# Kernel tuning notes

Measured on AMD Instinct MI355X. Metric: run time of the kernel, lower is better.

## Reference

```python
import jax, jax.numpy as jnp
import numpy as np
import math

EPS = 1e-6          # eps for safe cumprod / clamping
CHUNK = 4           # chunk_size w
SHARP = 1.0         # sharpening_factor
NOISE_STD = 1.0
N_HEADS = 4
ADIM = 512


def moving_sum(x, back, forward):
    """Windowed running sum over last axis: out[k] = sum_{j=k-back}^{k+forward} x[j].
    Equivalent to the conv1d trick in the original (all-ones filter)."""
    k = x.shape[-1]
    pad = [(0, 0)] * (x.ndim - 1) + [(back, forward)]
    c = jnp.cumsum(jnp.pad(x, pad), axis=-1)
    c0 = jnp.concatenate([jnp.zeros_like(c[..., :1]), c], axis=-1)
    w = back + forward
    return c0[..., w + 1: w + 1 + k] - c0[..., :k]


def setup_inputs() -> dict:
    rng = jax.random.key(0)
    ks = jax.random.split(rng, 12)
    B, qlen, klen, kdim, qdim, adim = 8, 256, 2048, 512, 512, ADIM
    s = 0.02
    return {
        "key_enc": jax.random.normal(ks[0], (B, klen, kdim), jnp.float32),
        "query":   jax.random.normal(ks[1], (B, qlen, qdim), jnp.float32),
        "noise":   jax.random.normal(ks[2], (B, qlen, klen), jnp.float32),
        # monotonic energy params
        "Wk_m": jax.random.normal(ks[3], (kdim, adim), jnp.float32) * s,
        "bk_m": jnp.zeros((adim,), jnp.float32),
        "Wq_m": jax.random.normal(ks[4], (qdim, adim), jnp.float32) * s,
        "bq_m": jnp.zeros((adim,), jnp.float32),
        "r":    jnp.array([-4.0], jnp.float32),
        # chunkwise energy params (multi-head)
        "Wk_c": jax.random.normal(ks[5], (kdim, adim), jnp.float32) * s,
        "bk_c": jnp.zeros((adim,), jnp.float32),
        "Wq_c": jax.random.normal(ks[6], (qdim, adim), jnp.float32) * s,
        "bq_c": jnp.zeros((adim,), jnp.float32),
    }


def _mocha_beta(key_enc, query, noise, Wk_m, bk_m, Wq_m, bq_m, r,
                Wk_c, bk_c, Wq_c, bq_c):
    B, klen, _ = key_enc.shape
    qlen = query.shape[1]
    H = N_HEADS
    dk = ADIM // H
    scale = math.sqrt(ADIM)

    # --- monotonic energy (single head): [B, qlen, klen]
    k_m = key_enc @ Wk_m + bk_m
    q_m = query @ Wq_m + bq_m
    e_mono = jnp.einsum('bqa,bka->bqk', q_m, k_m) / scale + r[0]

    # --- p_choose with additive gaussian noise (encourages discreteness)
    p_choose = jax.nn.sigmoid(e_mono + noise * NOISE_STD)  # [B,q,k]

    # --- safe cumprod of (1 - p) via exclusive cumsum in log space
    log1mp = jnp.log(jnp.clip(1.0 - p_choose, EPS, 1.0))
    cumprod_1mp = jnp.exp(jnp.cumsum(log1mp, axis=-1) - log1mp)  # exclusive

    # --- monotonic alpha recurrence over query steps (parallel-mode MoChA)
    aw0 = jnp.zeros((B, klen), jnp.float32).at[:, 0].set(1.0)

    def step(aw_prev, inp):
        p_i, cp_i = inp  # [B, klen]
        alpha_i = p_i * cp_i * jnp.cumsum(
            aw_prev / jnp.clip(cp_i, EPS, 1.0), axis=-1)
        return alpha_i, alpha_i

    xs = (jnp.swapaxes(p_choose, 0, 1), jnp.swapaxes(cumprod_1mp, 0, 1))
    _, alpha_q = jax.lax.scan(step, aw0, xs)          # [q, B, k]
    alpha = jnp.swapaxes(alpha_q, 0, 1)                # [B, q, k]

    # --- chunkwise energy (multi-head): [B, H, q, k]
    k_c = (key_enc @ Wk_c + bk_c).reshape(B, klen, H, dk)
    q_c = (query @ Wq_c + bq_c).reshape(B, qlen, H, dk)
    e_chunk = jnp.einsum('bqhd,bkhd->bhqk', q_c, k_c) / scale

    # --- efficient chunkwise attention (clipped-logit moving-sum softmax)
    e = e_chunk - jnp.max(e_chunk, axis=3, keepdims=True)
    softmax_exp = jnp.maximum(jnp.exp(e), 1e-5)
    denom = moving_sum(softmax_exp, back=CHUNK - 1, forward=0)
    beta = softmax_exp * moving_sum(
        alpha[:, None] * SHARP / denom, back=0, forward=CHUNK - 1)
    return beta  # [B, H, q, k]


def reference(key_enc, query, noise, Wk_m, bk_m, Wq_m, bq_m, r,
              Wk_c, bk_c, Wq_c, bq_c):
    return _mocha_beta(key_enc, query, noise, Wk_m, bk_m, Wq_m, bq_m, r,
                       Wk_c, bk_c, Wq_c, bq_c)
```

## Files before the change

kernel.cpp:

```cpp
#include <hip/hip_runtime.h>
#include <math.h>

#define BATCH   8
#define QLEN    256
#define KLEN    2048
#define KDIM    512
#define ADIMC   512
#define NHEADS  4
#define DKH     128
#define CHUNKW  4

static constexpr float INV_SCALE = 0.04419417382415922f;
static constexpr float EPSV = 1e-6f;

typedef __attribute__((ext_vector_type(8))) short bf16x8;
typedef __attribute__((ext_vector_type(4))) float f32x4;

__device__ __forceinline__ unsigned short f2bf(float f) {
    unsigned u = __builtin_bit_cast(unsigned, f);
    u += 0x7fffu + ((u >> 16) & 1u);
    return (unsigned short)(u >> 16);
}

__device__ __forceinline__ void lds_barrier() {
    __asm__ volatile("s_waitcnt lgkmcnt(0)\n\ts_barrier" ::: "memory");
}

__device__ __forceinline__ void gload_lds16(const void* g, void* l) {
    __builtin_amdgcn_global_load_lds(
        (const __attribute__((address_space(1))) void*)g,
        (__attribute__((address_space(3))) void*)l, 16, 0, 0);
}

__global__ __launch_bounds__(256) void cast_bf16(
    const float* __restrict__ x, unsigned short* __restrict__ y, int n4)
{
    int i = blockIdx.x * 256 + threadIdx.x;
    if (i < n4) {
        float4 v = ((const float4*)x)[i];
        ushort4 o;
        o.x = f2bf(v.x); o.y = f2bf(v.y); o.z = f2bf(v.z); o.w = f2bf(v.w);
        ((ushort4*)y)[i] = o;
    }
}

__global__ __launch_bounds__(256) void transpose_cast(
    const float* __restrict__ W, unsigned short* __restrict__ WT)
{
    __shared__ float tile[32][33];
    const int tx = threadIdx.x;
    const int ty = threadIdx.y;
    const int k0 = blockIdx.y * 32, n0 = blockIdx.x * 32;
    #pragma unroll
    for (int i = 0; i < 32; i += 8)
        tile[ty + i][tx] = W[(size_t)(k0 + ty + i) * KDIM + n0 + tx];
    __syncthreads();
    #pragma unroll
    for (int i = 0; i < 32; i += 8)
        WT[(size_t)(n0 + ty + i) * KDIM + k0 + tx] = f2bf(tile[tx][ty + i]);
}

template<int KSTEPS>
__device__ __forceinline__ void mfma_nt_staged(
    const unsigned short* __restrict__ A, const unsigned short* __restrict__ B,
    int lda, int ldb, int bm, int bn,
    unsigned short* AsLDS, unsigned short* BsLDS, f32x4 acc[4][4])
{
    const int t = threadIdx.x;
    const int wv = t >> 6, ln = t & 63;
    const int r = ln & 15, quad = ln >> 4;
    const int wm = (wv >> 1) * 64, wn = (wv & 1) * 64;
    const int srow = wv * 16 + (ln >> 2);
    const int scol = (ln & 3) * 8;

    for (int ks = 0; ks < KSTEPS; ++ks) {
        const int k0 = ks * 32;
        #pragma unroll
        for (int j = 0; j < 2; ++j) {
            gload_lds16(A + (size_t)(bm + j * 64 + srow) * lda + k0 + scol,
                        AsLDS + (size_t)(j * 64 + wv * 16) * 32);
            gload_lds16(B + (size_t)(bn + j * 64 + srow) * ldb + k0 + scol,
                        BsLDS + (size_t)(j * 64 + wv * 16) * 32);
        }
        __syncthreads();
        bf16x8 af[4], bg[4];
        #pragma unroll
        for (int f = 0; f < 4; ++f)
            af[f] = *(const bf16x8*)(AsLDS + (size_t)(wm + f * 16 + r) * 32 + quad * 8);
        #pragma unroll
        for (int f = 0; f < 4; ++f)
            bg[f] = *(const bf16x8*)(BsLDS + (size_t)(wn + f * 16 + r) * 32 + quad * 8);
        #pragma unroll
        for (int i = 0; i < 4; ++i)
            #pragma unroll
            for (int j2 = 0; j2 < 4; ++j2)
                acc[i][j2] = __builtin_amdgcn_mfma_f32_16x16x32_bf16(
                    af[i], bg[j2], acc[i][j2], 0, 0, 0);
        __syncthreads();
    }
}

__device__ __forceinline__ void zero_acc(f32x4 acc[4][4]) {
    #pragma unroll
    for (int i = 0; i < 4; ++i)
        #pragma unroll
        for (int j = 0; j < 4; ++j)
            acc[i][j] = f32x4{0.f, 0.f, 0.f, 0.f};
}

__global__ __launch_bounds__(256) void proj_mfma(
    const unsigned short* __restrict__ A, const unsigned short* __restrict__ WT,
    const float* __restrict__ bias_m, const float* __restrict__ bias_c,
    unsigned short* __restrict__ C)
{
    __shared__ unsigned short As[128 * 32];
    __shared__ unsigned short Bs[128 * 32];
    const int bm = blockIdx.y * 128, bn = blockIdx.x * 128;
    f32x4 acc[4][4]; zero_acc(acc);
    mfma_nt_staged<16>(A, WT, KDIM, KDIM, bm, bn, As, Bs, acc);
    const int wv = threadIdx.x >> 6, ln = threadIdx.x & 63;
    const int r = ln & 15, quad = ln >> 4;
    const int m0 = bm + (wv >> 1) * 64, n0 = bn + (wv & 1) * 64;
    #pragma unroll
    for (int j = 0; j < 4; ++j) {
        const int n = n0 + j * 16 + r;
        const float bv = (n < 512) ? bias_m[n] : bias_c[n - 512];
        #pragma unroll
        for (int i = 0; i < 4; ++i) {
            #pragma unroll
            for (int reg = 0; reg < 4; ++reg) {
                const int m = m0 + i * 16 + quad * 4 + reg;
                C[(size_t)m * 1024 + n] = f2bf(acc[i][j][reg] + bv);
            }
        }
    }
}

__global__ __launch_bounds__(256) void pchoose_mfma(
    const unsigned short* __restrict__ qp, const unsigned short* __restrict__ kp,
    const float* __restrict__ noise, const float* __restrict__ rp,
    float* __restrict__ p)
{
    __shared__ unsigned short As[128 * 32];
    __shared__ unsigned short Bs[128 * 32];
    const int b = blockIdx.z;
    const unsigned short* A = qp + (size_t)b * QLEN * 1024;
    const unsigned short* B = kp + (size_t)b * KLEN * 1024;
    const int bm = blockIdx.y * 128, bn = blockIdx.x * 128;
    f32x4 acc[4][4]; zero_acc(acc);
    mfma_nt_staged<16>(A, B, 1024, 1024, bm, bn, As, Bs, acc);
    const int wv = threadIdx.x >> 6, ln = threadIdx.x & 63;
    const int r = ln & 15, quad = ln >> 4;
    const int m0 = bm + (wv >> 1) * 64, n0 = bn + (wv & 1) * 64;
    const float rv = rp[0];
    #pragma unroll
    for (int i = 0; i < 4; ++i) {
        #pragma unroll
        for (int reg = 0; reg < 4; ++reg) {
            const int q = m0 + i * 16 + quad * 4 + reg;
            const size_t rowoff = ((size_t)b * QLEN + q) * KLEN;
            #pragma unroll
            for (int j = 0; j < 4; ++j) {
                const int k = n0 + j * 16 + r;
                const float e = acc[i][j][reg] * INV_SCALE + rv + noise[rowoff + k];
                p[rowoff + k] = __builtin_amdgcn_rcpf(1.0f + __expf(-e));
            }
        }
    }
}

__device__ __forceinline__ float wave_incl_scan(float x)
{
#define DPP_ADD(ctrl, rmask, bctrl)                                            \
    { int _t = __builtin_amdgcn_update_dpp(0, __builtin_bit_cast(int, x),      \
                                           ctrl, rmask, 0xf, bctrl);           \
      x += __builtin_bit_cast(float, _t); }
    DPP_ADD(0x111, 0xf, true)
    DPP_ADD(0x112, 0xf, true)
    DPP_ADD(0x114, 0xf, true)
    DPP_ADD(0x118, 0xf, true)
    DPP_ADD(0x142, 0xa, false)
    DPP_ADD(0x143, 0xc, false)
#undef DPP_ADD
    return x;
}

__global__ __launch_bounds__(256) void cumprod_mr(
    const float* __restrict__ p, float* __restrict__ mArr, float* __restrict__ rArr)
{
    const size_t row = blockIdx.x;
    const float* pr = p + row * KLEN;
    float* mr = mArr + row * KLEN;
    float* rr = rArr + row * KLEN;
    const int tid = threadIdx.x;
    const int lane = tid & 63, wid = tid >> 6;
    __shared__ float waveTot[4];

    float4 v0 = *(const float4*)(pr + tid * 8);
    float4 v1 = *(const float4*)(pr + tid * 8 + 4);
    float pv[8] = {v0.x, v0.y, v0.z, v0.w, v1.x, v1.y, v1.z, v1.w};
    float excl[8];
    float run = 0.0f;
    #pragma unroll
    for (int j = 0; j < 8; ++j) {
        float l = __logf(fminf(fmaxf(1.0f - pv[j], EPSV), 1.0f));
        excl[j] = run;
        run += l;
    }
    float s = wave_incl_scan(run);
    if (lane == 63) waveTot[wid] = s;
    __syncthreads();
    float wex = 0.0f;
    for (int w = 0; w < wid; ++w) wex += waveTot[w];
    const float texcl = wex + s - run;

    float mv[8], rv[8];
    #pragma unroll
    for (int j = 0; j < 8; ++j) {
        const float cpv = __expf(texcl + excl[j]);
        mv[j] = pv[j] * cpv;
        rv[j] = __builtin_amdgcn_rcpf(fminf(fmaxf(cpv, EPSV), 1.0f));
    }
    *(float4*)(mr + tid * 8)     = *(float4*)&mv[0];
    *(float4*)(mr + tid * 8 + 4) = *(float4*)&mv[4];
    *(float4*)(rr + tid * 8)     = *(float4*)&rv[0];
    *(float4*)(rr + tid * 8 + 4) = *(float4*)&rv[4];
}

__global__ __launch_bounds__(512, 1) void alpha_echunk(
    const float* __restrict__ mArr, const float* __restrict__ rArr,
    float* __restrict__ alpha,
    const unsigned short* __restrict__ qp, const unsigned short* __restrict__ kp,
    float* __restrict__ out)
{
    __shared__ __align__(16) char smem[16384];
    const int bid = blockIdx.x;
    const int tid = threadIdx.x;

    if (bid < BATCH) {
        float (*wt)[8] = (float (*)[8])smem;
        const int lane = tid & 63, wid = tid >> 6;
        const float* mrow = mArr + (size_t)bid * QLEN * KLEN + tid * 4;
        const float* rrow = rArr + (size_t)bid * QLEN * KLEN + tid * 4;
        float* arow = alpha + (size_t)bid * QLEN * KLEN + tid * 4;

        float aw0 = 0.f, aw1 = 0.f, aw2 = 0.f, aw3 = 0.f;
        if (tid == 0) aw0 = 1.0f;

        float4 mA = *(const float4*)(mrow);
        float4 rA = *(const float4*)(rrow);
        float4 mB = *(const float4*)(mrow + KLEN);
        float4 rB = *(const float4*)(rrow + KLEN);

#define ASTEP(I, MREG, RREG)                                                   \
    {                                                                          \
        const int i_ = (I);                                                    \
        float4 mc = MREG, rc = RREG;                                           \
        const int rn_ = (i_ + 2 < QLEN) ? (i_ + 2) : (QLEN - 1);               \
        MREG = *(const float4*)(mrow + (size_t)rn_ * KLEN);                    \
        RREG = *(const float4*)(rrow + (size_t)rn_ * KLEN);                    \
        float run = 0.0f, i0, i1, i2, i3;                                      \
        run = fmaf(aw0, rc.x, run); i0 = run;                                  \
        run = fmaf(aw1, rc.y, run); i1 = run;                                  \
        run = fmaf(aw2, rc.z, run); i2 = run;                                  \
        run = fmaf(aw3, rc.w, run); i3 = run;                                  \
        float tot = wave_incl_scan(run);                                       \
        if (lane == 63) wt[i_ & 1][wid] = tot;                                 \
        lds_barrier();                                                         \
        float base = tot - run;                                                \
        float4 w0 = *(const float4*)&wt[i_ & 1][0];                            \
        float4 w1 = *(const float4*)&wt[i_ & 1][4];                            \
        if (wid > 0) base += w0.x;                                             \
        if (wid > 1) base += w0.y;                                             \
        if (wid > 2) base += w0.z;                                             \
        if (wid > 3) base += w0.w;                                             \
        if (wid > 4) base += w1.x;                                             \
        if (wid > 5) base += w1.y;                                             \
        if (wid > 6) base += w1.z;                                             \
        aw0 = mc.x * (base + i0);                                              \
        aw1 = mc.y * (base + i1);                                              \
        aw2 = mc.z * (base + i2);                                              \
        aw3 = mc.w * (base + i3);                                              \
        float4 ov; ov.x = aw0; ov.y = aw1; ov.z = aw2; ov.w = aw3;             \
        *(float4*)(arow + (size_t)i_ * KLEN) = ov;                             \
    }

        for (int io = 0; io < QLEN; io += 2) {
            ASTEP(io + 0, mA, rA)
            ASTEP(io + 1, mB, rB)
        }
#undef ASTEP
        return;
    }

    const int v = bid - BATCH;
    const int z = v >> 5;
    const int by = (v >> 4) & 1;
    const int bx = v & 15;
    const int b = z >> 2, h = z & 3;
    const bool worker = tid < 256;
    unsigned short* As = (unsigned short*)smem;
    unsigned short* Bs = (unsigned short*)(smem + 8192);
    const unsigned short* A = qp + (size_t)b * QLEN * 1024 + 512 + h * DKH;
    const unsigned short* B = kp + (size_t)b * KLEN * 1024 + 512 + h * DKH;
    const int bm = by * 128, bn = bx * 128;

    const int wv = tid >> 6, ln = tid & 63;
    const int r = ln & 15, quad = ln >> 4;
    const int wm = (wv >> 1) * 64, wn = (wv & 1) * 64;
    const int srow = (wv & 3) * 16 + (ln >> 2);
    const int scol = (ln & 3) * 8;

    f32x4 acc[4][4]; zero_acc(acc);
    for (int ks = 0; ks < 4; ++ks) {
        const int k0 = ks * 32;
        if (worker) {
            #pragma unroll
            for (int j = 0; j < 2; ++j) {
                gload_lds16(A + (size_t)(bm + j * 64 + srow) * 1024 + k0 + scol,
                            As + (size_t)(j * 64 + wv * 16) * 32);
                gload_lds16(B + (size_t)(bn + j * 64 + srow) * 1024 + k0 + scol,
                            Bs + (size_t)(j * 64 + wv * 16) * 32);
            }
        }
        __syncthreads();
        if (worker) {
            bf16x8 af[4], bg[4];
            #pragma unroll
            for (int f = 0; f < 4; ++f)
                af[f] = *(const bf16x8*)(As + (size_t)(wm + f * 16 + r) * 32 + quad * 8);
            #pragma unroll
            for (int f = 0; f < 4; ++f)
                bg[f] = *(const bf16x8*)(Bs + (size_t)(wn + f * 16 + r) * 32 + quad * 8);
            #pragma unroll
            for (int i = 0; i < 4; ++i)
                #pragma unroll
                for (int j2 = 0; j2 < 4; ++j2)
                    acc[i][j2] = __builtin_amdgcn_mfma_f32_16x16x32_bf16(
                        af[i], bg[j2], acc[i][j2], 0, 0, 0);
        }
        __syncthreads();
    }
    if (worker) {
        const int m0 = bm + (wv >> 1) * 64, n0 = bn + (wv & 1) * 64;
        #pragma unroll
        for (int i = 0; i < 4; ++i) {
            #pragma unroll
            for (int reg = 0; reg < 4; ++reg) {
                const int q = m0 + i * 16 + quad * 4 + reg;
                const size_t rowoff = ((size_t)z * QLEN + q) * KLEN;
                #pragma unroll
                for (int j = 0; j < 4; ++j) {
                    const int k = n0 + j * 16 + r;
                    out[rowoff + k] = acc[i][j][reg] * INV_SCALE;
                }
            }
        }
    }
}

__global__ __launch_bounds__(256) void beta_kernel(
    float* __restrict__ eo, const float* __restrict__ alpha)
{
    __shared__ float sse[KLEN + 3];
    __shared__ float su[KLEN + 3];
    __shared__ float wmax[4];

    const int tid = threadIdx.x;
    const int lane = tid & 63, wid = tid >> 6;
    const int row = blockIdx.x;
    const int q = row & (QLEN - 1);
    const int b = row >> 10;
    float* erow = eo + (size_t)row * KLEN;
    const float* arow = alpha + ((size_t)b * QLEN + q) * KLEN;

    if (tid < 3) { sse[tid] = 0.0f; su[KLEN + tid] = 0.0f; }

    float ev[8];
    float lm = -INFINITY;
    #pragma unroll
    for (int j = 0; j < 8; ++j) {
        const int k = tid + 256 * j;
        ev[j] = erow[k];
        lm = fmaxf(lm, ev[j]);
    }
    #pragma unroll
    for (int off = 32; off > 0; off >>= 1) lm = fmaxf(lm, __shfl_xor(lm, off));
    if (lane == 0) wmax[wid] = lm;
    __syncthreads();
    const float mx = fmaxf(fmaxf(wmax[0], wmax[1]), fmaxf(wmax[2], wmax[3]));

    #pragma unroll
    for (int j = 0; j < 8; ++j) {
        const int k = tid + 256 * j;
        sse[k + 3] = fmaxf(__expf(ev[j] - mx), 1e-5f);
    }
    __syncthreads();

    #pragma unroll
    for (int j = 0; j < 8; ++j) {
        const int k = tid + 256 * j;
        const float denom = sse[k + 3] + sse[k + 2] + sse[k + 1] + sse[k];
        su[k] = arow[k] * __builtin_amdgcn_rcpf(denom);
    }
    __syncthreads();

    #pragma unroll
    for (int j = 0; j < 8; ++j) {
        const int k = tid + 256 * j;
        erow[k] = sse[k + 3] * (su[k] + su[k + 1] + su[k + 2] + su[k + 3]);
    }
}

extern "C" void kernel_launch(void* const* d_in, const int* in_sizes, int n_in,
                              void* d_out, int out_size, void* d_ws, size_t ws_size,
                              hipStream_t stream)
{
    (void)in_sizes; (void)n_in; (void)out_size; (void)ws_size;
    const float* key_enc = (const float*)d_in[0];
    const float* query   = (const float*)d_in[1];
    const float* noise   = (const float*)d_in[2];
    const float* Wk_m    = (const float*)d_in[3];
    const float* bk_m    = (const float*)d_in[4];
    const float* Wq_m    = (const float*)d_in[5];
    const float* bq_m    = (const float*)d_in[6];
    const float* rp      = (const float*)d_in[7];
    const float* Wk_c    = (const float*)d_in[8];
    const float* bk_c    = (const float*)d_in[9];
    const float* Wq_c    = (const float*)d_in[10];
    const float* bq_c    = (const float*)d_in[11];
    float* out = (float*)d_out;

    char* w = (char*)d_ws;
    unsigned short* kx    = (unsigned short*)w; w += (size_t)BATCH * KLEN * KDIM * 2;
    unsigned short* qx    = (unsigned short*)w; w += (size_t)BATCH * QLEN * KDIM * 2;
    unsigned short* WTk   = (unsigned short*)w; w += (size_t)1024 * KDIM * 2;
    unsigned short* WTq   = (unsigned short*)w; w += (size_t)1024 * KDIM * 2;
    unsigned short* kproj = (unsigned short*)w; w += (size_t)BATCH * KLEN * 1024 * 2;
    unsigned short* qproj = (unsigned short*)w; w += (size_t)BATCH * QLEN * 1024 * 2;
    float* p_alpha = (float*)w; w += (size_t)BATCH * QLEN * KLEN * 4;
    float* mArr    = (float*)w; w += (size_t)BATCH * QLEN * KLEN * 4;
    float* rArr    = (float*)w;

    hipLaunchKernelGGL(cast_bf16, dim3(BATCH * KLEN * KDIM / 4 / 256), dim3(256), 0, stream,
                       key_enc, kx, BATCH * KLEN * KDIM / 4);
    hipLaunchKernelGGL(cast_bf16, dim3(BATCH * QLEN * KDIM / 4 / 256), dim3(256), 0, stream,
                       query, qx, BATCH * QLEN * KDIM / 4);
    hipLaunchKernelGGL(transpose_cast, dim3(16, 16), dim3(32, 8), 0, stream, Wk_m, WTk);
    hipLaunchKernelGGL(transpose_cast, dim3(16, 16), dim3(32, 8), 0, stream, Wk_c, WTk + (size_t)512 * KDIM);
    hipLaunchKernelGGL(transpose_cast, dim3(16, 16), dim3(32, 8), 0, stream, Wq_m, WTq);
    hipLaunchKernelGGL(transpose_cast, dim3(16, 16), dim3(32, 8), 0, stream, Wq_c, WTq + (size_t)512 * KDIM);

    hipLaunchKernelGGL(proj_mfma, dim3(8, BATCH * KLEN / 128), dim3(256), 0, stream,
                       kx, WTk, bk_m, bk_c, kproj);
    hipLaunchKernelGGL(proj_mfma, dim3(8, BATCH * QLEN / 128), dim3(256), 0, stream,
                       qx, WTq, bq_m, bq_c, qproj);

    hipLaunchKernelGGL(pchoose_mfma, dim3(KLEN / 128, QLEN / 128, BATCH), dim3(256), 0, stream,
                       qproj, kproj, noise, rp, p_alpha);

    hipLaunchKernelGGL(cumprod_mr, dim3(BATCH * QLEN), dim3(256), 0, stream,
                       p_alpha, mArr, rArr);

    hipLaunchKernelGGL(alpha_echunk, dim3(BATCH + KLEN / 128 * QLEN / 128 * BATCH * NHEADS),
                       dim3(512), 0, stream,
                       mArr, rArr, p_alpha, qproj, kproj, out);

    hipLaunchKernelGGL(beta_kernel, dim3(BATCH * NHEADS * QLEN), dim3(256), 0, stream,
                       out, p_alpha);
}
```

Measured before the change: 313.6 us.

## Run alpha scan with a single wave per batch to drop block barriers

After: 1.008 ms. 221% more time.

```diff
diff --git a/kernel.cpp b/kernel.cpp
--- a/kernel.cpp
+++ b/kernel.cpp
@@ -20,10 +20,6 @@
     unsigned u = __builtin_bit_cast(unsigned, f);
     u += 0x7fffu + ((u >> 16) & 1u);
     return (unsigned short)(u >> 16);
-}
-
-__device__ __forceinline__ void lds_barrier() {
-    __asm__ volatile("s_waitcnt lgkmcnt(0)\n\ts_barrier" ::: "memory");
 }
 
 __device__ __forceinline__ void gload_lds16(const void* g, void* l) {
@@ -238,58 +234,103 @@
     const int tid = threadIdx.x;
 
     if (bid < BATCH) {
-        float (*wt)[8] = (float (*)[8])smem;
-        const int lane = tid & 63, wid = tid >> 6;
-        const float* mrow = mArr + (size_t)bid * QLEN * KLEN + tid * 4;
-        const float* rrow = rArr + (size_t)bid * QLEN * KLEN + tid * 4;
-        float* arow = alpha + (size_t)bid * QLEN * KLEN + tid * 4;
-
-        float aw0 = 0.f, aw1 = 0.f, aw2 = 0.f, aw3 = 0.f;
-        if (tid == 0) aw0 = 1.0f;
-
-        float4 mA = *(const float4*)(mrow);
-        float4 rA = *(const float4*)(rrow);
-        float4 mB = *(const float4*)(mrow + KLEN);
-        float4 rB = *(const float4*)(rrow + KLEN);
-
-#define ASTEP(I, MREG, RREG)                                                   \
+        if (tid >= 64) return;
+        const int l = tid;
+        const size_t rowbase = (size_t)bid * QLEN * KLEN + (size_t)l * 32;
+        const float* mb = mArr + rowbase;
+        const float* rb = rArr + rowbase;
+        float* ab = alpha + rowbase;
+
+        float4 aw[8];
+        #pragma unroll
+        for (int j = 0; j < 8; ++j) aw[j] = float4{0.f, 0.f, 0.f, 0.f};
+        if (l == 0) aw[0].x = 1.0f;
+
+        float4 mA[8], rA[8], mB[8], rB[8];
+        #pragma unroll
+        for (int j = 0; j < 8; ++j) {
+            mA[j] = *(const float4*)(mb + 4 * j);
+            rA[j] = *(const float4*)(rb + 4 * j);
+            mB[j] = *(const float4*)(mb + KLEN + 4 * j);
+            rB[j] = *(const float4*)(rb + KLEN + 4 * j);
+        }
+
+#define GRP(c, J0, J1, RC)                                                     \
+        c = fmaf(aw[J0].x, RC[J0].x, c); aw[J0].x = c;                         \
+        c = fmaf(aw[J0].y, RC[J0].y, c); aw[J0].y = c;                         \
+        c = fmaf(aw[J0].z, RC[J0].z, c); aw[J0].z = c;                         \
+        c = fmaf(aw[J0].w, RC[J0].w, c); aw[J0].w = c;                         \
+        c = fmaf(aw[J1].x, RC[J1].x, c); aw[J1].x = c;                         \
+        c = fmaf(aw[J1].y, RC[J1].y, c); aw[J1].y = c;                         \
+        c = fmaf(aw[J1].z, RC[J1].z, c); aw[J1].z = c;                         \
+        c = fmaf(aw[J1].w, RC[J1].w, c); aw[J1].w = c;
+
+#define EPI(J0, J1, MC, Bg)                                                    \
+        aw[J0].x = MC[J0].x * (Bg + aw[J0].x);                                 \
+        aw[J0].y = MC[J0].y * (Bg + aw[J0].y);                                 \
+        aw[J0].z = MC[J0].z * (Bg + aw[J0].z);                                 \
+        aw[J0].w = MC[J0].w * (Bg + aw[J0].w);                                 \
+        aw[J1].x = MC[J1].x * (Bg + aw[J1].x);                                 \
+        aw[J1].y = MC[J1].y * (Bg + aw[J1].y);                                 \
+        aw[J1].z = MC[J1].z * (Bg + aw[J1].z);                                 \
+        aw[J1].w = MC[J1].w * (Bg + aw[J1].w);
+
+#define A1(I, MC, RC)                                                          \
     {                                                                          \
         const int i_ = (I);                                                    \
-        float4 mc = MREG, rc = RREG;                                           \
+        float t0 = 0.f, t1 = 0.f, t2 = 0.f, t3 = 0.f;                          \
+        GRP(t0, 0, 1, RC)                                                      \
+        GRP(t1, 2, 3, RC)                                                      \
+        GRP(t2, 4, 5, RC)                                                      \
+        GRP(t3, 6, 7, RC)                                                      \
+        const float o1 = t0, o2 = o1 + t1, o3 = o2 + t2;                       \
+        float run = o3 + t3;                                                   \
+              \
         const int rn_ = (i_ + 2 < QLEN) ? (i_ + 2) : (QLEN - 1);               \
-        MREG = *(const float4*)(mrow + (size_t)rn_ * KLEN);                    \
-        RREG = *(const float4*)(rrow + (size_t)rn_ * KLEN);                    \
-        float run = 0.0f, i0, i1, i2, i3;                                      \
-        run = fmaf(aw0, rc.x, run); i0 = run;                                  \
-        run = fmaf(aw1, rc.y, run); i1 = run;                                  \
-        run = fmaf(aw2, rc.z, run); i2 = run;                                  \
-        run = fmaf(aw3, rc.w, run); i3 = run;                                  \
-        float tot = wave_incl_scan(run);                                       \
-        if (lane == 63) wt[i_ & 1][wid] = tot;                                 \
-        lds_barrier();                                                         \
-        float base = tot - run;                                                \
-        float4 w0 = *(const float4*)&wt[i_ & 1][0];                            \
-        float4 w1 = *(const float4*)&wt[i_ & 1][4];                            \
-        if (wid > 0) base += w0.x;                                             \
-        if (wid > 1) base += w0.y;                                             \
-        if (wid > 2) base += w0.z;                                             \
-        if (wid > 3) base += w0.w;                                             \
-        if (wid > 4) base += w1.x;                                             \
-        if (wid > 5) base += w1.y;                                             \
-        if (wid > 6) base += w1.z;                                             \
-        aw0 = mc.x * (base + i0);                                              \
-        aw1 = mc.y * (base + i1);                                              \
-        aw2 = mc.z * (base + i2);                                              \
-        aw3 = mc.w * (base + i3);                                              \
-        float4 ov; ov.x = aw0; ov.y = aw1; ov.z = aw2; ov.w = aw3;             \
-        *(float4*)(arow + (size_t)i_ * KLEN) = ov;                             \
+        const float* rbn = rb + (size_t)rn_ * KLEN;                            \
+        RC[0] = *(const float4*)(rbn);                                         \
+        RC[1] = *(const float4*)(rbn + 4);                                     \
+        RC[2] = *(const float4*)(rbn + 8);                                     \
+        RC[3] = *(const float4*)(rbn + 12);                                    \
+        RC[4] = *(const float4*)(rbn + 16);                                    \
+        RC[5] = *(const float4*)(rbn + 20);                                    \
+        RC[6] = *(const float4*)(rbn + 24);                                    \
+        RC[7] = *(const float4*)(rbn + 28);                                    \
+        const float s_ = wave_incl_scan(run);                                  \
+        const float base = s_ - run;                                           \
+        const float B0 = base, B1 = base + o1, B2 = base + o2, B3 = base + o3; \
+        EPI(0, 1, MC, B0)                                                      \
+        EPI(2, 3, MC, B1)                                                      \
+        EPI(4, 5, MC, B2)                                                      \
+        EPI(6, 7, MC, B3)                                                      \
+        float* ao = ab + (size_t)i_ * KLEN;                                    \
+        *(float4*)(ao)      = aw[0];                                           \
+        *(float4*)(ao + 4)  = aw[1];                                           \
+        *(float4*)(ao + 8)  = aw[2];                                           \
+        *(float4*)(ao + 12) = aw[3];                                           \
+        *(float4*)(ao + 16) = aw[4];                                           \
+        *(float4*)(ao + 20) = aw[5];                                           \
+        *(float4*)(ao + 24) = aw[6];                                           \
+        *(float4*)(ao + 28) = aw[7];                                           \
+                                  \
+        const float* mbn = mb + (size_t)rn_ * KLEN;                            \
+        MC[0] = *(const float4*)(mbn);                                         \
+        MC[1] = *(const float4*)(mbn + 4);                                     \
+        MC[2] = *(const float4*)(mbn + 8);                                     \
+        MC[3] = *(const float4*)(mbn + 12);                                    \
+        MC[4] = *(const float4*)(mbn + 16);                                    \
+        MC[5] = *(const float4*)(mbn + 20);                                    \
+        MC[6] = *(const float4*)(mbn + 24);                                    \
+        MC[7] = *(const float4*)(mbn + 28);                                    \
     }
 
         for (int io = 0; io < QLEN; io += 2) {
-            ASTEP(io + 0, mA, rA)
-            ASTEP(io + 1, mB, rB)
-        }
-#undef ASTEP
+            A1(io + 0, mA, rA)
+            A1(io + 1, mB, rB)
+        }
+#undef A1
+#undef EPI
+#undef GRP
         return;
     }
 
```
